# Optimization experiments

Hardware: AMD Instinct MI355X
Metric: run time of the kernel (lower is better)

## Reference

```python
import jax, jax.numpy as jnp
import numpy as np

# Config (mirrors HymbaLayer init + env constants)
DIM = 1024; NH = 16; NKV = 4; D = 64          # head_dim = DIM // NH
NATTN = NH // 2; NSSM = NH // 2; KVREP = NATTN // NKV
S = 16          # _HYMBA_SSM_STATE
NMETA = 4       # _HYMBA_META_TOK
BASE = 10000.0  # rope_base
CHUNK = 64      # _HYMBA_SCAN_CHUNK
B, T = 2, 2048


def _rms_norm(x, eps=1e-6):
    return x * jax.lax.rsqrt(jnp.mean(x * x, -1, keepdims=True) + eps)


def _rotary_cs(t_len, d, base):
    inv = 1.0 / (base ** (jnp.arange(0, d, 2, dtype=jnp.float32) / d))  # (d/2,)
    f = jnp.arange(t_len, dtype=jnp.float32)[:, None] * inv[None, :]    # (T, d/2)
    return jnp.cos(f), jnp.sin(f)


def _apply_rot(x, cos, sin):
    # x: (B, H, T, D); rotate-half style rotary
    d2 = x.shape[-1] // 2
    x1, x2 = x[..., :d2], x[..., d2:]
    c, s = cos[None, None], sin[None, None]
    return jnp.concatenate([x1 * c - x2 * s, x1 * s + x2 * c], -1)


def _scan_chunks(log_a, u, chunk):
    # Exact chunk-parallel diagonal scan: h_t = exp(log_a_t)*h_{t-1} + u_t
    b, t, s = u.shape
    nc = t // chunk
    la = log_a.reshape(b, nc, chunk, s)
    uu = u.reshape(b, nc, chunk, s)
    log_p = jnp.clip(jnp.cumsum(la, axis=2), -30.0, 0.0)
    p = jnp.exp(log_p)
    h_local = p * jnp.cumsum(uu * jnp.exp(-log_p), axis=2)

    def step(h0, args):
        hl, pc = args                          # (B, chunk, S)
        hc = hl + pc * h0[:, None, :]
        return hc[:, -1], hc

    _, hs = jax.lax.scan(step, jnp.zeros((b, s), u.dtype),
                         (jnp.swapaxes(h_local, 0, 1), jnp.swapaxes(p, 0, 1)))
    return jnp.swapaxes(hs, 0, 1).reshape(b, t, s)


def _mamba_head(logA, Bw, Cw, dtw, dtb, Ow, x):
    # x: (B, T, D); selective SSM with diagonal A
    dt = jnp.minimum(jax.nn.softplus(x @ dtw.T + dtb), 1.0)   # (B,T,S)
    A = jnp.minimum(-jnp.exp(logA), 10.0)                      # (S,)
    log_a = jnp.clip(dt * A, -0.5, 0.0)
    Bx = (x @ Bw.T) * dt
    Cc = x @ Cw.T
    h = _scan_chunks(log_a, Bx, CHUNK)                         # (B,T,S)
    y = jnp.sum(Cc * h, -1, keepdims=True)
    return h @ Ow.T + y * x[..., :1]


def _forward(x, meta_tokens, c_q_w, c_k_w, c_v_w, q_gain, ssm_in_w, proj_w,
             attn_scale, ssm_scale, ssm_logA, ssm_Bw, ssm_Cw, ssm_dtw, ssm_dtb, ssm_Ow):
    b, t, c = x.shape
    x_ext = jnp.concatenate([jnp.broadcast_to(meta_tokens, (b, NMETA, c)), x], 1)
    t_ext = t + NMETA
    q = (x_ext @ c_q_w.T).reshape(b, t_ext, NH, D).transpose(0, 2, 1, 3)
    k = (x_ext @ c_k_w.T).reshape(b, t_ext, NKV, D).transpose(0, 2, 1, 3)
    v = (x_ext @ c_v_w.T).reshape(b, t_ext, NKV, D).transpose(0, 2, 1, 3)
    q = _rms_norm(q); k = _rms_norm(k)
    cos, sin = _rotary_cs(t_ext, D, BASE)
    q = _apply_rot(q, cos, sin); k = _apply_rot(k, cos, sin)
    # GQA attention over the first NATTN heads, causal over T_ext
    q_attn = q[:, :NATTN] * q_gain[None, :, None, None]
    k_exp = jnp.repeat(k, KVREP, axis=1)
    v_exp = jnp.repeat(v, KVREP, axis=1)
    scores = jnp.einsum('bhqd,bhkd->bhqk', q_attn, k_exp) / jnp.sqrt(jnp.float32(D))
    mask = jnp.tril(jnp.ones((t_ext, t_ext), bool))
    scores = jnp.where(mask[None, None], scores, -jnp.inf)
    attn = jax.nn.softmax(scores, axis=-1)
    ao = jnp.einsum('bhqk,bhkd->bhqd', attn, v_exp)
    ao = ao[:, :, NMETA:].transpose(0, 2, 1, 3).reshape(b, t, NATTN * D) * attn_scale
    # SSM branch on the original (un-prepended) tokens
    ssm_x = (x @ ssm_in_w.T).reshape(b, t, NSSM, D)
    ssm_out = jax.vmap(_mamba_head, in_axes=(0, 0, 0, 0, 0, 0, 2), out_axes=2)(
        ssm_logA, ssm_Bw, ssm_Cw, ssm_dtw, ssm_dtb, ssm_Ow, ssm_x)
    ssm_out = ssm_out.reshape(b, t, NSSM * D) * ssm_scale
    return jnp.concatenate([ao, ssm_out], -1) @ proj_w.T


def setup_inputs() -> dict:
    key = jax.random.key(0)
    ks = jax.random.split(key, 16)
    r = lambda k, sh, sc=0.02: jax.random.normal(k, sh, jnp.float32) * sc
    return {
        'x': jax.random.normal(ks[0], (B, T, DIM), jnp.float32),
        'meta_tokens': r(ks[1], (1, NMETA, DIM)),
        'c_q_w': r(ks[2], (DIM, DIM)),
        'c_k_w': r(ks[3], (NKV * D, DIM)),
        'c_v_w': r(ks[4], (NKV * D, DIM)),
        'q_gain': jnp.full((NATTN,), 1.0, jnp.float32),
        'ssm_in_w': r(ks[5], (NSSM * D, DIM)),
        'proj_w': r(ks[6], (DIM, DIM)),
        'attn_scale': jnp.ones((1,), jnp.float32),
        'ssm_scale': jnp.ones((1,), jnp.float32),
        'ssm_logA': jax.random.normal(ks[7], (NSSM, S), jnp.float32) * 0.5,
        'ssm_Bw': r(ks[8], (NSSM, S, D), 0.05),
        'ssm_Cw': r(ks[9], (NSSM, S, D), 0.05),
        'ssm_dtw': r(ks[10], (NSSM, S, D), 0.05),
        'ssm_dtb': jnp.full((NSSM, S), -4.0, jnp.float32),
        'ssm_Ow': r(ks[11], (NSSM, D, S), 0.05),
    }


def reference(x, meta_tokens, c_q_w, c_k_w, c_v_w, q_gain, ssm_in_w, proj_w,
              attn_scale, ssm_scale, ssm_logA, ssm_Bw, ssm_Cw, ssm_dtw, ssm_dtb, ssm_Ow):
    return _forward(x, meta_tokens, c_q_w, c_k_w, c_v_w, q_gain, ssm_in_w, proj_w,
                    attn_scale, ssm_scale, ssm_logA, ssm_Bw, ssm_Cw, ssm_dtw, ssm_dtb, ssm_Ow)
```

## Files before the change

kernel.cpp:

```cpp
#include <hip/hip_runtime.h>
#include <hip/hip_bf16.h>
#include <math.h>

typedef __hip_bfloat16 bf16;
typedef __attribute__((ext_vector_type(8))) short short8;
typedef __attribute__((ext_vector_type(4))) float f32x4;

static constexpr int kB = 2;
static constexpr int kT = 2048;
static constexpr int kDIM = 1024;
static constexpr int kNMETA = 4;
static constexpr int kTEXT = kT + kNMETA;
static constexpr int kMEXT = kB * kTEXT;
static constexpr int kMPAD = 4224;
static constexpr int kMX = kB * kT;
static constexpr int kQT = 33;
static constexpr int kTP = 2112;

static constexpr size_t oXE = 0;
static constexpr size_t oYB = 0;
static constexpr size_t oLU = 8650752;
static constexpr size_t oCC = oLU + (size_t)kMX * 128 * 8;
static constexpr size_t oHL = oCC + (size_t)kMX * 128 * 4;
static constexpr size_t oX0 = oHL + (size_t)kMX * 128 * 2;
static constexpr size_t oQP = oX0 + (size_t)kMX * 8 * 4;
static constexpr size_t oKP = oQP + (size_t)kB * 8 * kTP * 64 * 2;
static constexpr size_t oVT = oKP + (size_t)kB * 4 * kTP * 64 * 2;
static constexpr size_t oWP = oVT + (size_t)kB * 4 * 64 * kTP * 2;
static constexpr size_t oWQ = oWP + (size_t)1024 * 1024 * 2;
static constexpr size_t oAO = 134217728;
static constexpr size_t oAL = oAO + (size_t)3 * kB * 8 * kTP * 64 * 2;

#define GLD_LDS16(gp, lp)                                                          \
  __builtin_amdgcn_global_load_lds((const __attribute__((address_space(1))) void*)(gp), \
                                   (__attribute__((address_space(3))) void*)(lp), 16, 0, 0)

__device__ __forceinline__ short bf2s(float f) {
  union { bf16 h; short s; } u;
  u.h = __float2bfloat16(f);
  return u.s;
}

__device__ __forceinline__ float bf2f(unsigned short u) {
  return __uint_as_float(((unsigned int)u) << 16);
}

__device__ __forceinline__ uint4 pack8(float4 a, float4 b) {
  union { bf16 h[8]; uint4 v; } u;
  u.h[0] = __float2bfloat16(a.x); u.h[1] = __float2bfloat16(a.y);
  u.h[2] = __float2bfloat16(a.z); u.h[3] = __float2bfloat16(a.w);
  u.h[4] = __float2bfloat16(b.x); u.h[5] = __float2bfloat16(b.y);
  u.h[6] = __float2bfloat16(b.z); u.h[7] = __float2bfloat16(b.w);
  return u.v;
}

__device__ __forceinline__ void add16bf(const bf16* p, float* o) {
  uint4 a = ((const uint4*)p)[0], b = ((const uint4*)p)[1];
  const unsigned short* s0 = (const unsigned short*)&a;
  const unsigned short* s1 = (const unsigned short*)&b;
#pragma unroll
  for (int i = 0; i < 8; ++i) { o[i] += bf2f(s0[i]); o[8 + i] += bf2f(s1[i]); }
}

__global__ __launch_bounds__(256) void prep_all(const float* __restrict__ cq, const float* __restrict__ ck,
                                                const float* __restrict__ cv, const float* __restrict__ sw,
                                                const float* __restrict__ pw,
                                                const float* __restrict__ x, const float* __restrict__ meta,
                                                bf16* __restrict__ wqkvsx, bf16* __restrict__ wproj,
                                                bf16* __restrict__ xe,
                                                bf16* __restrict__ Qp, bf16* __restrict__ Kp,
                                                bf16* __restrict__ Vt) {
  int i = blockIdx.x * 256 + threadIdx.x;
  if (i < 327680) {
    int row = i >> 7, v = i & 127;
    const float* src; bf16* dst;
    if (row < 512)       { src = cq + (size_t)row * 1024;          dst = wqkvsx + (size_t)row * 1024; }
    else if (row < 768)  { src = ck + (size_t)(row - 512) * 1024;  dst = wqkvsx + (size_t)row * 1024; }
    else if (row < 1024) { src = cv + (size_t)(row - 768) * 1024;  dst = wqkvsx + (size_t)row * 1024; }
    else if (row < 1536) { src = sw + (size_t)(row - 1024) * 1024; dst = wqkvsx + (size_t)row * 1024; }
    else                 { src = pw + (size_t)(row - 1536) * 1024; dst = wproj + (size_t)(row - 1536) * 1024; }
    float4 a0 = ((const float4*)src)[v * 2], a1 = ((const float4*)src)[v * 2 + 1];
    ((uint4*)dst)[v] = pack8(a0, a1);
  } else if (i < 868352) {
    int j = i - 327680;
    int r = j >> 7, v = j & 127;
    uint4 val = {0u, 0u, 0u, 0u};
    if (r < kMEXT) {
      int b = r / kTEXT, te = r - b * kTEXT;
      const float* src = (te < kNMETA) ? (meta + (size_t)te * kDIM)
                                       : (x + ((size_t)b * kT + (te - kNMETA)) * kDIM);
      float4 a0 = ((const float4*)src)[v * 2];
      float4 a1 = ((const float4*)src)[v * 2 + 1];
      val = pack8(a0, a1);
    }
    ((uint4*)(xe + (size_t)r * kDIM))[v] = val;
  } else {
    int j = i - 868352;
    if (j < 30720) {
      int k = j & 31, te = (j >> 5) % 60, bh = j / (60 * 32);
      *(unsigned int*)(Qp + ((size_t)bh * kTP + 2052 + te) * 64 + k * 2) = 0u;
    } else if (j < 46080) {
      int jj = j - 30720;
      int k = jj & 31, te = (jj >> 5) % 60, bh = jj / (60 * 32);
      *(unsigned int*)(Kp + ((size_t)bh * kTP + 2052 + te) * 64 + k * 2) = 0u;
    } else if (j < 61440) {
      int jj = j - 46080;
      int k = jj % 30, rowd = jj / 30;
      *(unsigned int*)(Vt + (size_t)rowd * kTP + 2052 + k * 2) = 0u;
    }
  }
}

template <int MODE>
__global__ __launch_bounds__(256) void gemm_t(const bf16* __restrict__ A,
                                              const bf16* __restrict__ W,
                                              void* __restrict__ O0, void* __restrict__ O1,
                                              void* __restrict__ O2,
                                              const float* __restrict__ q_gain,
                                              const float* __restrict__ dtw, const float* __restrict__ dtb,
                                              const float* __restrict__ Bw, const float* __restrict__ Cw,
                                              const float* __restrict__ logA,
                                              float* __restrict__ LU, float* __restrict__ CC,
                                              float* __restrict__ X0) {
  __shared__ char smem[49152];
  const int tid = threadIdx.x;
  const int wave = tid >> 6, lane = tid & 63;
  const int quad = lane >> 4, l16 = lane & 15;
  const int bm = blockIdx.y * 128, bn = blockIdx.x * 64;
  const bf16* ag0 = A + (size_t)(bm + (tid >> 2)) * 1024 + (tid & 3) * 8;
  const bf16* ag1 = A + (size_t)(bm + 64 + (tid >> 2)) * 1024 + (tid & 3) * 8;
  const bf16* bg0 = W + (size_t)(bn + (tid >> 2)) * 1024 + (tid & 3) * 8;
  f32x4 acc[2][4] = {};
  {
    char* sb = smem + wave * 1024;
    GLD_LDS16(ag0, sb);
    GLD_LDS16(ag1, sb + 4096);
    GLD_LDS16(ag0 + 32, sb + 8192);
    GLD_LDS16(ag1 + 32, sb + 12288);
    GLD_LDS16(bg0, sb + 16384);
    GLD_LDS16(bg0 + 32, sb + 20480);
    ag0 += 64; ag1 += 64; bg0 += 64;
  }
  for (int k = 0; k < 16; ++k) {
    char* cur = smem + (k & 1) * 24576;
    char* nxt = smem + ((k & 1) ^ 1) * 24576;
    __syncthreads();
    if (k < 15) {
      char* sb = nxt + wave * 1024;
      GLD_LDS16(ag0, sb);
      GLD_LDS16(ag1, sb + 4096);
      GLD_LDS16(ag0 + 32, sb + 8192);
      GLD_LDS16(ag1 + 32, sb + 12288);
      GLD_LDS16(bg0, sb + 16384);
      GLD_LDS16(bg0 + 32, sb + 20480);
      ag0 += 64; ag1 += 64; bg0 += 64;
    }
#pragma unroll
    for (int p = 0; p < 2; ++p) {
      short8 af[2], bfr[4];
#pragma unroll
      for (int mi = 0; mi < 2; ++mi)
        af[mi] = *(const short8*)(cur + p * 8192 +
                                  (size_t)(wave * 32 + mi * 16 + l16) * 64 + quad * 16);
#pragma unroll
      for (int ni = 0; ni < 4; ++ni)
        bfr[ni] = *(const short8*)(cur + 16384 + p * 4096 +
                                   (size_t)(ni * 16 + l16) * 64 + quad * 16);
#pragma unroll
      for (int mi = 0; mi < 2; ++mi)
#pragma unroll
        for (int ni = 0; ni < 4; ++ni)
          acc[mi][ni] = __builtin_amdgcn_mfma_f32_16x16x32_bf16(af[mi], bfr[ni], acc[mi][ni], 0, 0, 0);
    }
  }
  if constexpr (MODE == 2) {
#pragma unroll
    for (int mi = 0; mi < 2; ++mi)
#pragma unroll
      for (int ni = 0; ni < 4; ++ni) {
        int colg = bn + ni * 16 + l16;
#pragma unroll
        for (int r = 0; r < 4; ++r) {
          int row = bm + wave * 32 + mi * 16 + quad * 4 + r;
          ((float*)O0)[(size_t)row * 1024 + colg] = acc[mi][ni][r];
        }
      }
  } else {
    const int tile = blockIdx.x;
    if (tile < 16) {
      float gain = (tile < 8) ? q_gain[tile] * 0.125f : 1.f;
      float inv0 = exp2f(-13.287712379549449f * (float)l16 * (1.f / 32.f));
      float inv1 = exp2f(-13.287712379549449f * (float)(l16 + 16) * (1.f / 32.f));
#pragma unroll
      for (int mi = 0; mi < 2; ++mi) {
        int row0 = bm + wave * 32 + mi * 16 + quad * 4;
        if (row0 >= kMEXT) continue;
        int b = row0 >= kTEXT ? 1 : 0;
        int te0 = row0 - b * kTEXT;
        if (tile < 12) {
          float ss[4];
#pragma unroll
          for (int r = 0; r < 4; ++r) {
            float s = 0.f;
#pragma unroll
            for (int ni = 0; ni < 4; ++ni) s += acc[mi][ni][r] * acc[mi][ni][r];
#pragma unroll
            for (int off = 1; off < 16; off <<= 1) s += __shfl_xor(s, off, 64);
            ss[r] = s;
          }
          bf16* base = (tile < 8)
            ? (bf16*)O0 + (((size_t)(b * 8 + tile)) * kTP + te0) * 64 + l16
            : (bf16*)O1 + (((size_t)(b * 4 + tile - 8)) * kTP + te0) * 64 + l16;
#pragma unroll
          for (int r = 0; r < 4; ++r) {
            float rn = rsqrtf(ss[r] * (1.f / 64.f) + 1e-6f) * gain;
            float te = (float)(te0 + r);
            float a0 = te * inv0, a1 = te * inv1;
            float c0 = __cosf(a0), s0 = __sinf(a0);
            float c1 = __cosf(a1), s1 = __sinf(a1);
            float v0 = acc[mi][0][r] * rn, v1 = acc[mi][1][r] * rn;
            float v2 = acc[mi][2][r] * rn, v3 = acc[mi][3][r] * rn;
            bf16* dst = base + (size_t)r * 64;
            dst[0]  = __float2bfloat16(v0 * c0 - v2 * s0);
            dst[16] = __float2bfloat16(v1 * c1 - v3 * s1);
            dst[32] = __float2bfloat16(v0 * s0 + v2 * c0);
            dst[48] = __float2bfloat16(v1 * s1 + v3 * c1);
          }
        } else {
          int hv = tile - 12;
#pragma unroll
          for (int ni = 0; ni < 4; ++ni) {
            union { unsigned long long q; bf16 hh[4]; } pw;
#pragma unroll
            for (int r = 0; r < 4; ++r) pw.hh[r] = __float2bfloat16(acc[mi][ni][r]);
            *(unsigned long long*)((bf16*)O2 +
                (((size_t)(b * 4 + hv)) * 64 + ni * 16 + l16) * kTP + te0) = pw.q;
          }
        }
      }
    } else {
      const int hd = tile - 16;
      __syncthreads();
      short (*Xl)[72] = (short(*)[72])smem;
      short (*Wl)[72] = (short(*)[72])(smem + 18432);
#pragma unroll
      for (int mi = 0; mi < 2; ++mi) {
        if (l16 == 0) {
#pragma unroll
          for (int r = 0; r < 4; ++r) {
            int row = bm + wave * 32 + mi * 16 + quad * 4 + r;
            if (row < kMEXT) {
              int bb = row >= kTEXT ? 1 : 0;
              int te = row - bb * kTEXT;
              if (te >= kNMETA) X0[(size_t)(bb * kT + te - kNMETA) * 8 + hd] = acc[mi][0][r];
            }
          }
        }
      }
#pragma unroll
      for (int mi = 0; mi < 2; ++mi)
#pragma unroll
        for (int ni = 0; ni < 4; ++ni)
#pragma unroll
          for (int r = 0; r < 4; ++r)
            Xl[wave * 32 + mi * 16 + quad * 4 + r][ni * 16 + l16] = bf2s(acc[mi][ni][r]);
      for (int s2 = tid; s2 < 384; s2 += 256) {
        int row = s2 >> 3, v = s2 & 7;
        const float* src = (row < 16) ? dtw + ((size_t)(hd * 16 + row)) * 64
                         : (row < 32) ? Bw + ((size_t)(hd * 16 + row - 16)) * 64
                                      : Cw + ((size_t)(hd * 16 + row - 32)) * 64;
        float4 a0 = ((const float4*)src)[v * 2];
        float4 a1 = ((const float4*)src)[v * 2 + 1];
        *(uint4*)&Wl[row][v * 8] = pack8(a0, a1);
      }
      __syncthreads();
      f32x4 a3[2][3] = {};
#pragma unroll
      for (int mt = 0; mt < 2; ++mt) {
        short8 xa0 = *(const short8*)&Xl[wave * 32 + mt * 16 + l16][quad * 8];
        short8 xa1 = *(const short8*)&Xl[wave * 32 + mt * 16 + l16][32 + quad * 8];
#pragma unroll
        for (int nb = 0; nb < 3; ++nb) {
          short8 wb0 = *(const short8*)&Wl[nb * 16 + l16][quad * 8];
          a3[mt][nb] = __builtin_amdgcn_mfma_f32_16x16x32_bf16(xa0, wb0, a3[mt][nb], 0, 0, 0);
          short8 wb1 = *(const short8*)&Wl[nb * 16 + l16][32 + quad * 8];
          a3[mt][nb] = __builtin_amdgcn_mfma_f32_16x16x32_bf16(xa1, wb1, a3[mt][nb], 0, 0, 0);
        }
      }
      float dtb_v = dtb[hd * 16 + l16];
      float A_v = fminf(-expf(logA[hd * 16 + l16]), 10.f);
#pragma unroll
      for (int mt = 0; mt < 2; ++mt)
#pragma unroll
        for (int r = 0; r < 4; ++r) {
          int row = bm + wave * 32 + mt * 16 + quad * 4 + r;
          if (row >= kMEXT) continue;
          int bb = row >= kTEXT ? 1 : 0;
          int te = row - bb * kTEXT;
          if (te < kNMETA) continue;
          size_t ix = (size_t)(bb * kT + te - kNMETA) * 128 + hd * 16 + l16;
          float raw = a3[mt][0][r] + dtb_v;
          float sp = fmaxf(raw, 0.f) + log1pf(expf(-fabsf(raw)));
          float dt = fminf(sp, 1.f);
          float lav = fminf(fmaxf(dt * A_v, -0.5f), 0.f);
          *(float2*)(LU + 2 * ix) = make_float2(lav, a3[mt][1][r] * dt);
          CC[ix] = a3[mt][2][r];
        }
    }
  }
}

__global__ __launch_bounds__(256) void attn_scan(const bf16* __restrict__ Qp,
                                                 const bf16* __restrict__ Kp,
                                                 const bf16* __restrict__ Vt,
                                                 bf16* __restrict__ AO, float* __restrict__ AL,
                                                 const float* __restrict__ LU, bf16* __restrict__ HL) {
  __shared__ char sraw[27648];
  if (blockIdx.x < 64) {
    float (*sH)[64] = (float(*)[64])sraw;
    float (*sP)[64] = (float(*)[64])(sraw + 1024);
    float (*sH0)[64] = (float(*)[64])(sraw + 2048);
    const int tid = threadIdx.x;
    const int ch = tid & 3, c = tid >> 2;
    const int chain = blockIdx.x * 4 + ch;
    const int b = chain >> 7, hs = chain & 127;
    const float2* LU2 = (const float2*)LU;
    const size_t base = ((size_t)b * kT) * 128 + hs;
    float H = 0.f, cum = 0.f;
    for (int i = 0; i < 32; ++i) {
      float2 lu = LU2[base + (size_t)(c * 32 + i) * 128];
      cum += lu.x;
      H = __expf(lu.x) * H + lu.y;
    }
    sH[ch][c] = H;
    sP[ch][c] = __expf(cum);
    __syncthreads();
    const int wv = tid >> 6, lane = tid & 63;
    float Hs = sH[wv][lane], Ps = sP[wv][lane];
#pragma unroll
    for (int off = 1; off < 64; off <<= 1) {
      float Hp = __shfl_up(Hs, off, 64);
      float Pp = __shfl_up(Ps, off, 64);
      if (lane >= off) { Hs = Hs + Ps * Hp; Ps = Ps * Pp; }
    }
    float Hex = __shfl_up(Hs, 1, 64);
    if (lane == 0) Hex = 0.f;
    sH0[wv][lane] = Hex;
    __syncthreads();
    float h = sH0[ch][c];
    for (int i = 0; i < 32; ++i) {
      size_t ix = base + (size_t)(c * 32 + i) * 128;
      float2 lu = LU2[ix];
      h = __expf(lu.x) * h + lu.y;
      HL[ix] = __float2bfloat16(h);
    }
    return;
  }
  short (*Ks)[72] = (short(*)[72])sraw;
  short (*Vs)[72] = (short(*)[72])(sraw + 9216);
  short (*Ps)[16][72] = (short(*)[16][72])(sraw + 18432);
  const int i = blockIdx.x - 64;
  const int xq = i % 99;
  const int h = (i / 99) & 7, b = i / 792;
  const int part = xq % 3;
  const int qt = (kQT - 1) - (xq / 3);
  const int kvh = h >> 1;
  const int tid = threadIdx.x, wave = tid >> 6, lane = tid & 63;
  const int quad = lane >> 4, l16 = lane & 15;
  const int ntiles = qt + 1;
  const int s1 = ntiles / 3, s2 = (2 * ntiles) / 3;
  const int kt_begin = (part == 0) ? 0 : (part == 1 ? s1 : s2);
  const int kt_end = (part == 0) ? s1 : (part == 1 ? s2 : ntiles);
  if (kt_begin >= kt_end) return;

  short8 qf[2];
  {
    const bf16* qrow = Qp + (((size_t)(b * 8 + h)) * kTP + qt * 64 + wave * 16 + l16) * 64 + quad * 8;
    qf[0] = *(const short8*)(qrow);
    qf[1] = *(const short8*)(qrow + 32);
  }
  short8 ones;
#pragma unroll
  for (int j = 0; j < 8; ++j) ones[j] = (short)0x3F80;

  const bf16* kbase = Kp + ((size_t)(b * 4 + kvh)) * kTP * 64;
  const bf16* vbase = Vt + ((size_t)(b * 4 + kvh)) * 64 * kTP;

  const int r0row = tid >> 3, r0c8 = tid & 7;
  const int r1row = (256 + tid) >> 3, r1c8 = tid & 7;

  f32x4 O[4] = {};
  f32x4 lacc = {};
  const int q_abs = qt * 64 + wave * 16 + l16;

  uint4 kr0 = *(const uint4*)(kbase + (size_t)(kt_begin * 64 + r0row) * 64 + r0c8 * 8);
  uint4 kr1 = *(const uint4*)(kbase + (size_t)(kt_begin * 64 + r1row) * 64 + r1c8 * 8);
  uint4 vr0 = *(const uint4*)(vbase + (size_t)r0row * kTP + kt_begin * 64 + r0c8 * 8);
  uint4 vr1 = *(const uint4*)(vbase + (size_t)r1row * kTP + kt_begin * 64 + r1c8 * 8);

  for (int kt = kt_begin; kt < kt_end; ++kt) {
    __syncthreads();
    *(uint4*)&Ks[r0row][r0c8 * 8] = kr0;
    *(uint4*)&Ks[r1row][r1c8 * 8] = kr1;
    *(uint4*)&Vs[r0row][r0c8 * 8] = vr0;
    *(uint4*)&Vs[r1row][r1c8 * 8] = vr1;
    if (kt + 1 < kt_end) {
      int kn = (kt + 1) * 64;
      kr0 = *(const uint4*)(kbase + (size_t)(kn + r0row) * 64 + r0c8 * 8);
      kr1 = *(const uint4*)(kbase + (size_t)(kn + r1row) * 64 + r1c8 * 8);
      vr0 = *(const uint4*)(vbase + (size_t)r0row * kTP + kn + r0c8 * 8);
      vr1 = *(const uint4*)(vbase + (size_t)r1row * kTP + kn + r1c8 * 8);
    }
    __syncthreads();

    f32x4 st[4] = {};
#pragma unroll
    for (int nb = 0; nb < 4; ++nb) {
      short8 ak0 = *(const short8*)&Ks[nb * 16 + l16][quad * 8];
      st[nb] = __builtin_amdgcn_mfma_f32_16x16x32_bf16(ak0, qf[0], st[nb], 0, 0, 0);
      short8 ak1 = *(const short8*)&Ks[nb * 16 + l16][32 + quad * 8];
      st[nb] = __builtin_amdgcn_mfma_f32_16x16x32_bf16(ak1, qf[1], st[nb], 0, 0, 0);
    }
    if (kt == qt) {
      int key0 = kt * 64 + quad * 4;
#pragma unroll
      for (int nb = 0; nb < 4; ++nb)
#pragma unroll
        for (int rg = 0; rg < 4; ++rg)
          if (key0 + nb * 16 + rg > q_abs) st[nb][rg] = -1e30f;
    }
#pragma unroll
    for (int nb = 0; nb < 4; ++nb) {
      union { unsigned long long q; bf16 hh[4]; } pw;
#pragma unroll
      for (int rg = 0; rg < 4; ++rg) pw.hh[rg] = __float2bfloat16(__expf(st[nb][rg]));
      *(unsigned long long*)&Ps[wave][l16][nb * 16 + quad * 4] = pw.q;
    }
    short8 pf0 = *(const short8*)&Ps[wave][l16][quad * 8];
    short8 pf1 = *(const short8*)&Ps[wave][l16][32 + quad * 8];
    lacc = __builtin_amdgcn_mfma_f32_16x16x32_bf16(pf0, ones, lacc, 0, 0, 0);
    lacc = __builtin_amdgcn_mfma_f32_16x16x32_bf16(pf1, ones, lacc, 0, 0, 0);
#pragma unroll
    for (int db = 0; db < 4; ++db) {
      short8 bv0 = *(const short8*)&Vs[db * 16 + l16][quad * 8];
      O[db] = __builtin_amdgcn_mfma_f32_16x16x32_bf16(pf0, bv0, O[db], 0, 0, 0);
      short8 bv1 = *(const short8*)&Vs[db * 16 + l16][32 + quad * 8];
      O[db] = __builtin_amdgcn_mfma_f32_16x16x32_bf16(pf1, bv1, O[db], 0, 0, 0);
    }
  }
  size_t hb = (((size_t)part * 2 + b) * 8 + h);
  bf16* aoB = AO + hb * kTP * 64;
  float* alB = AL + hb * kTP;
#pragma unroll
  for (int rg = 0; rg < 4; ++rg) {
    int q = qt * 64 + wave * 16 + quad * 4 + rg;
    bf16* dst = aoB + (size_t)q * 64 + l16;
#pragma unroll
    for (int db = 0; db < 4; ++db) dst[db * 16] = __float2bfloat16(O[db][rg]);
    if (l16 == 0) alB[q] = lacc[rg];
  }
}

__global__ __launch_bounds__(256) void combine_out(const bf16* __restrict__ AO,
                                                   const float* __restrict__ AL,
                                                   const float* __restrict__ attn_scale,
                                                   const bf16* __restrict__ HL, const float* __restrict__ CC,
                                                   const float* __restrict__ X0, const float* __restrict__ Ow,
                                                   const float* __restrict__ ssm_scale,
                                                   bf16* __restrict__ Y) {
  if (blockIdx.x < 528) {
    int id = blockIdx.x * 256 + threadIdx.x;
    int d16 = id & 3;
    int tmp = id >> 2;
    int q = tmp % kTP; tmp /= kTP;
    int h = tmp & 7, b = tmp >> 3;
    if (q < kNMETA || q >= kTEXT) return;
    int ntiles = (q >> 6) + 1;
    bool use0 = ntiles >= 3, use1 = ntiles >= 2;
    size_t hb0 = ((size_t)b * 8 + h), hb1 = ((size_t)(2 + b) * 8 + h), hb2 = ((size_t)(4 + b) * 8 + h);
    float l = (use0 ? AL[hb0 * kTP + q] : 0.f) + (use1 ? AL[hb1 * kTP + q] : 0.f) + AL[hb2 * kTP + q];
    float so = attn_scale[0] / fmaxf(l, 1e-30f);
    float ov[16];
#pragma unroll
    for (int j = 0; j < 16; ++j) ov[j] = 0.f;
    if (use0) add16bf(AO + (hb0 * kTP + q) * 64 + d16 * 16, ov);
    if (use1) add16bf(AO + (hb1 * kTP + q) * 64 + d16 * 16, ov);
    add16bf(AO + (hb2 * kTP + q) * 64 + d16 * 16, ov);
    bf16* dst = Y + ((size_t)(b * kT + q - kNMETA)) * kDIM + h * 64 + d16 * 16;
#pragma unroll
    for (int j = 0; j < 16; ++j) dst[j] = __float2bfloat16(ov[j] * so);
  } else {
    int id = (blockIdx.x - 528) * 256 + threadIdx.x;
    int d4 = id & 3, h = (id >> 2) & 7, t = (id >> 5) & 2047, b = id >> 16;
    size_t ix0 = ((size_t)(b * kT + t)) * 128 + h * 16;
    float hv[16], y = 0.f;
#pragma unroll
    for (int s = 0; s < 16; ++s) {
      float v = __bfloat162float(HL[ix0 + s]);
      hv[s] = v;
      y += CC[ix0 + s] * v;
    }
    float x0 = X0[(size_t)(b * kT + t) * 8 + h];
    float scl = ssm_scale[0];
    const float* ow = Ow + ((size_t)h * 64 + d4 * 16) * 16;
    bf16* dst = Y + ((size_t)(b * kT + t)) * kDIM + 512 + h * 64 + d4 * 16;
    float yx = y * x0;
#pragma unroll
    for (int d = 0; d < 16; ++d) {
      float acc = yx;
      const float* owr = ow + d * 16;
#pragma unroll
      for (int s = 0; s < 16; ++s) acc += hv[s] * owr[s];
      dst[d] = __float2bfloat16(acc * scl);
    }
  }
}

extern "C" void kernel_launch(void* const* d_in, const int* in_sizes, int n_in,
                              void* d_out, int out_size, void* d_ws, size_t ws_size,
                              hipStream_t stream) {
  (void)in_sizes; (void)n_in; (void)out_size; (void)ws_size;
  const float* x        = (const float*)d_in[0];
  const float* meta     = (const float*)d_in[1];
  const float* c_q_w    = (const float*)d_in[2];
  const float* c_k_w    = (const float*)d_in[3];
  const float* c_v_w    = (const float*)d_in[4];
  const float* q_gain   = (const float*)d_in[5];
  const float* ssm_in_w = (const float*)d_in[6];
  const float* proj_w   = (const float*)d_in[7];
  const float* attn_sc  = (const float*)d_in[8];
  const float* ssm_sc   = (const float*)d_in[9];
  const float* ssm_logA = (const float*)d_in[10];
  const float* ssm_Bw   = (const float*)d_in[11];
  const float* ssm_Cw   = (const float*)d_in[12];
  const float* ssm_dtw  = (const float*)d_in[13];
  const float* ssm_dtb  = (const float*)d_in[14];
  const float* ssm_Ow   = (const float*)d_in[15];

  char* w = (char*)d_ws;
  bf16*  XE = (bf16*)(w + oXE);
  bf16*  YB = (bf16*)(w + oYB);
  bf16*  QP = (bf16*)(w + oQP);
  bf16*  KP = (bf16*)(w + oKP);
  bf16*  VT = (bf16*)(w + oVT);
  bf16*  WQ = (bf16*)(w + oWQ);
  bf16*  WP = (bf16*)(w + oWP);
  float* LU = (float*)(w + oLU);
  float* CC = (float*)(w + oCC);
  bf16*  HL = (bf16*)(w + oHL);
  float* X0 = (float*)(w + oX0);
  bf16*  AO = (bf16*)(w + oAO);
  float* AL = (float*)(w + oAL);

  prep_all<<<3632, 256, 0, stream>>>(c_q_w, c_k_w, c_v_w, ssm_in_w, proj_w,
                                     x, meta, WQ, WP, XE, QP, KP, VT);

  gemm_t<0><<<dim3(24, kMPAD / 128), 256, 0, stream>>>(XE, WQ, QP, KP, VT, q_gain,
                                                       ssm_dtw, ssm_dtb, ssm_Bw, ssm_Cw,
                                                       ssm_logA, LU, CC, X0);

  attn_scan<<<64 + kQT * 3 * 8 * kB, 256, 0, stream>>>(QP, KP, VT, AO, AL, LU, HL);

  combine_out<<<1040, 256, 0, stream>>>(AO, AL, attn_sc, HL, CC, X0, ssm_Ow, ssm_sc, YB);

  gemm_t<2><<<dim3(16, kMX / 128), 256, 0, stream>>>(YB, WP, d_out, nullptr, nullptr, nullptr,
                                                     nullptr, nullptr, nullptr, nullptr, nullptr,
                                                     nullptr, nullptr, nullptr);
}
```

Before: 194.4 us.

## Process both GQA query heads per block sharing K/V tiles; split keys four ways

Each attention block now handles the two query heads that share one KV head, so every K/V tile loaded into LDS feeds twice as many MFMAs. The key range is split into four parts instead of three to keep enough blocks in flight, and the combine pass sums up to four partial outputs. This halves K/V global and LDS traffic per query head. In exchange it raises register pressure from doubled accumulators and serialises the P staging through LDS per head.

```diff
diff --git a/kernel.cpp b/kernel.cpp
--- a/kernel.cpp
+++ b/kernel.cpp
@@ -29,7 +29,7 @@
 static constexpr size_t oWP = oVT + (size_t)kB * 4 * 64 * kTP * 2;
 static constexpr size_t oWQ = oWP + (size_t)1024 * 1024 * 2;
 static constexpr size_t oAO = 134217728;
-static constexpr size_t oAL = oAO + (size_t)3 * kB * 8 * kTP * 64 * 2;
+static constexpr size_t oAL = oAO + (size_t)4 * kB * 8 * kTP * 64 * 2;
 
 #define GLD_LDS16(gp, lp)                                                          \
   __builtin_amdgcn_global_load_lds((const __attribute__((address_space(1))) void*)(gp), \
@@ -360,24 +360,24 @@
   short (*Vs)[72] = (short(*)[72])(sraw + 9216);
   short (*Ps)[16][72] = (short(*)[16][72])(sraw + 18432);
   const int i = blockIdx.x - 64;
-  const int xq = i % 99;
-  const int h = (i / 99) & 7, b = i / 792;
-  const int part = xq % 3;
-  const int qt = (kQT - 1) - (xq / 3);
-  const int kvh = h >> 1;
+  const int xq = i % 132;
+  const int kvh = (i / 132) & 3, b = i / 528;
+  const int part = xq & 3;
+  const int qt = (kQT - 1) - (xq >> 2);
+  const int h0 = kvh * 2;
   const int tid = threadIdx.x, wave = tid >> 6, lane = tid & 63;
   const int quad = lane >> 4, l16 = lane & 15;
   const int ntiles = qt + 1;
-  const int s1 = ntiles / 3, s2 = (2 * ntiles) / 3;
-  const int kt_begin = (part == 0) ? 0 : (part == 1 ? s1 : s2);
-  const int kt_end = (part == 0) ? s1 : (part == 1 ? s2 : ntiles);
+  const int kt_begin = (part * ntiles) >> 2;
+  const int kt_end = ((part + 1) * ntiles) >> 2;
   if (kt_begin >= kt_end) return;
 
-  short8 qf[2];
-  {
-    const bf16* qrow = Qp + (((size_t)(b * 8 + h)) * kTP + qt * 64 + wave * 16 + l16) * 64 + quad * 8;
-    qf[0] = *(const short8*)(qrow);
-    qf[1] = *(const short8*)(qrow + 32);
+  short8 qf[2][2];
+#pragma unroll
+  for (int hh = 0; hh < 2; ++hh) {
+    const bf16* qrow = Qp + (((size_t)(b * 8 + h0 + hh)) * kTP + qt * 64 + wave * 16 + l16) * 64 + quad * 8;
+    qf[hh][0] = *(const short8*)(qrow);
+    qf[hh][1] = *(const short8*)(qrow + 32);
   }
   short8 ones;
 #pragma unroll
@@ -389,8 +389,8 @@
   const int r0row = tid >> 3, r0c8 = tid & 7;
   const int r1row = (256 + tid) >> 3, r1c8 = tid & 7;
 
-  f32x4 O[4] = {};
-  f32x4 lacc = {};
+  f32x4 O[2][4] = {};
+  f32x4 lacc[2] = {};
   const int q_abs = qt * 64 + wave * 16 + l16;
 
   uint4 kr0 = *(const uint4*)(kbase + (size_t)(kt_begin * 64 + r0row) * 64 + r0c8 * 8);
@@ -413,13 +413,16 @@
     }
     __syncthreads();
 
-    f32x4 st[4] = {};
+    f32x4 st[2][4] = {};
 #pragma unroll
     for (int nb = 0; nb < 4; ++nb) {
       short8 ak0 = *(const short8*)&Ks[nb * 16 + l16][quad * 8];
-      st[nb] = __builtin_amdgcn_mfma_f32_16x16x32_bf16(ak0, qf[0], st[nb], 0, 0, 0);
       short8 ak1 = *(const short8*)&Ks[nb * 16 + l16][32 + quad * 8];
-      st[nb] = __builtin_amdgcn_mfma_f32_16x16x32_bf16(ak1, qf[1], st[nb], 0, 0, 0);
+#pragma unroll
+      for (int hh = 0; hh < 2; ++hh) {
+        st[hh][nb] = __builtin_amdgcn_mfma_f32_16x16x32_bf16(ak0, qf[hh][0], st[hh][nb], 0, 0, 0);
+        st[hh][nb] = __builtin_amdgcn_mfma_f32_16x16x32_bf16(ak1, qf[hh][1], st[hh][nb], 0, 0, 0);
+      }
     }
     if (kt == qt) {
       int key0 = kt * 64 + quad * 4;
@@ -427,37 +430,47 @@
       for (int nb = 0; nb < 4; ++nb)
 #pragma unroll
         for (int rg = 0; rg < 4; ++rg)
-          if (key0 + nb * 16 + rg > q_abs) st[nb][rg] = -1e30f;
-    }
-#pragma unroll
-    for (int nb = 0; nb < 4; ++nb) {
-      union { unsigned long long q; bf16 hh[4]; } pw;
-#pragma unroll
-      for (int rg = 0; rg < 4; ++rg) pw.hh[rg] = __float2bfloat16(__expf(st[nb][rg]));
-      *(unsigned long long*)&Ps[wave][l16][nb * 16 + quad * 4] = pw.q;
-    }
-    short8 pf0 = *(const short8*)&Ps[wave][l16][quad * 8];
-    short8 pf1 = *(const short8*)&Ps[wave][l16][32 + quad * 8];
-    lacc = __builtin_amdgcn_mfma_f32_16x16x32_bf16(pf0, ones, lacc, 0, 0, 0);
-    lacc = __builtin_amdgcn_mfma_f32_16x16x32_bf16(pf1, ones, lacc, 0, 0, 0);
+          if (key0 + nb * 16 + rg > q_abs) { st[0][nb][rg] = -1e30f; st[1][nb][rg] = -1e30f; }
+    }
+    short8 pf[2][2];
+#pragma unroll
+    for (int hh = 0; hh < 2; ++hh) {
+#pragma unroll
+      for (int nb = 0; nb < 4; ++nb) {
+        union { unsigned long long q; bf16 hv4[4]; } pw;
+#pragma unroll
+        for (int rg = 0; rg < 4; ++rg) pw.hv4[rg] = __float2bfloat16(__expf(st[hh][nb][rg]));
+        *(unsigned long long*)&Ps[wave][l16][nb * 16 + quad * 4] = pw.q;
+      }
+      pf[hh][0] = *(const short8*)&Ps[wave][l16][quad * 8];
+      pf[hh][1] = *(const short8*)&Ps[wave][l16][32 + quad * 8];
+      lacc[hh] = __builtin_amdgcn_mfma_f32_16x16x32_bf16(pf[hh][0], ones, lacc[hh], 0, 0, 0);
+      lacc[hh] = __builtin_amdgcn_mfma_f32_16x16x32_bf16(pf[hh][1], ones, lacc[hh], 0, 0, 0);
+    }
 #pragma unroll
     for (int db = 0; db < 4; ++db) {
       short8 bv0 = *(const short8*)&Vs[db * 16 + l16][quad * 8];
-      O[db] = __builtin_amdgcn_mfma_f32_16x16x32_bf16(pf0, bv0, O[db], 0, 0, 0);
       short8 bv1 = *(const short8*)&Vs[db * 16 + l16][32 + quad * 8];
-      O[db] = __builtin_amdgcn_mfma_f32_16x16x32_bf16(pf1, bv1, O[db], 0, 0, 0);
-    }
-  }
-  size_t hb = (((size_t)part * 2 + b) * 8 + h);
-  bf16* aoB = AO + hb * kTP * 64;
-  float* alB = AL + hb * kTP;
-#pragma unroll
-  for (int rg = 0; rg < 4; ++rg) {
-    int q = qt * 64 + wave * 16 + quad * 4 + rg;
-    bf16* dst = aoB + (size_t)q * 64 + l16;
-#pragma unroll
-    for (int db = 0; db < 4; ++db) dst[db * 16] = __float2bfloat16(O[db][rg]);
-    if (l16 == 0) alB[q] = lacc[rg];
+#pragma unroll
+      for (int hh = 0; hh < 2; ++hh) {
+        O[hh][db] = __builtin_amdgcn_mfma_f32_16x16x32_bf16(pf[hh][0], bv0, O[hh][db], 0, 0, 0);
+        O[hh][db] = __builtin_amdgcn_mfma_f32_16x16x32_bf16(pf[hh][1], bv1, O[hh][db], 0, 0, 0);
+      }
+    }
+  }
+#pragma unroll
+  for (int hh = 0; hh < 2; ++hh) {
+    size_t hb = (((size_t)part * 2 + b) * 8 + h0 + hh);
+    bf16* aoB = AO + hb * kTP * 64;
+    float* alB = AL + hb * kTP;
+#pragma unroll
+    for (int rg = 0; rg < 4; ++rg) {
+      int q = qt * 64 + wave * 16 + quad * 4 + rg;
+      bf16* dst = aoB + (size_t)q * 64 + l16;
+#pragma unroll
+      for (int db = 0; db < 4; ++db) dst[db * 16] = __float2bfloat16(O[hh][db][rg]);
+      if (l16 == 0) alB[q] = lacc[hh][rg];
+    }
   }
 }
 
@@ -476,16 +489,19 @@
     int h = tmp & 7, b = tmp >> 3;
     if (q < kNMETA || q >= kTEXT) return;
     int ntiles = (q >> 6) + 1;
-    bool use0 = ntiles >= 3, use1 = ntiles >= 2;
-    size_t hb0 = ((size_t)b * 8 + h), hb1 = ((size_t)(2 + b) * 8 + h), hb2 = ((size_t)(4 + b) * 8 + h);
-    float l = (use0 ? AL[hb0 * kTP + q] : 0.f) + (use1 ? AL[hb1 * kTP + q] : 0.f) + AL[hb2 * kTP + q];
+    float l = 0.f;
+    float ov[16];
+#pragma unroll
+    for (int j = 0; j < 16; ++j) ov[j] = 0.f;
+#pragma unroll
+    for (int p = 0; p < 4; ++p) {
+      if (((p * ntiles) >> 2) < (((p + 1) * ntiles) >> 2)) {
+        size_t hb = (((size_t)p * 2 + b) * 8 + h);
+        l += AL[hb * kTP + q];
+        add16bf(AO + (hb * kTP + q) * 64 + d16 * 16, ov);
+      }
+    }
     float so = attn_scale[0] / fmaxf(l, 1e-30f);
-    float ov[16];
-#pragma unroll
-    for (int j = 0; j < 16; ++j) ov[j] = 0.f;
-    if (use0) add16bf(AO + (hb0 * kTP + q) * 64 + d16 * 16, ov);
-    if (use1) add16bf(AO + (hb1 * kTP + q) * 64 + d16 * 16, ov);
-    add16bf(AO + (hb2 * kTP + q) * 64 + d16 * 16, ov);
     bf16* dst = Y + ((size_t)(b * kT + q - kNMETA)) * kDIM + h * 64 + d16 * 16;
 #pragma unroll
     for (int j = 0; j < 16; ++j) dst[j] = __float2bfloat16(ov[j] * so);
@@ -559,7 +575,7 @@
                                                        ssm_dtw, ssm_dtb, ssm_Bw, ssm_Cw,
                                                        ssm_logA, LU, CC, X0);
 
-  attn_scan<<<64 + kQT * 3 * 8 * kB, 256, 0, stream>>>(QP, KP, VT, AO, AL, LU, HL);
+  attn_scan<<<64 + kQT * 4 * 4 * kB, 256, 0, stream>>>(QP, KP, VT, AO, AL, LU, HL);
 
   combine_out<<<1040, 256, 0, stream>>>(AO, AL, attn_sc, HL, CC, X0, ssm_Ow, ssm_sc, YB);
 
```

Result: no change. 193.1 us (-0.6%).
